# Performance work log

Hardware: AMD Instinct MI355X
Metric: run time of the kernel (lower is better)

The kernel has to match this reference:

```python
import jax, jax.numpy as jnp
import numpy as np

N = 8192          # number of nodes
D = 256           # node feature dim
OUT = 256         # output dim
AVG_DEG = 32      # target sparsity of adj (~AVG_DEG nonzeros per row)


def setup_inputs() -> dict:
    key = jax.random.key(0)
    k1, k2, k3, k4, k5 = jax.random.split(key, 5)
    node_features = jax.random.normal(k1, (N, D), dtype=jnp.float32)
    edge_features = jax.random.normal(k2, (N, N), dtype=jnp.float32)
    # sparse-ish adjacency: ~AVG_DEG nonzeros per row, stored dense (matches torch spmm math)
    u = jax.random.uniform(k3, (N, N), dtype=jnp.float32)
    adj = jnp.where(u < (AVG_DEG / N), 1.0, 0.0).astype(jnp.float32)
    stdv = 1.0 / np.sqrt(OUT)
    weight = jax.random.uniform(k4, (2 * D + 1, OUT), minval=-stdv, maxval=stdv, dtype=jnp.float32)
    bias = jax.random.uniform(k5, (OUT,), minval=-stdv, maxval=stdv, dtype=jnp.float32)
    return {"node_features": node_features, "edge_features": edge_features,
            "adj": adj, "weight": weight, "bias": bias}


def reference(node_features, edge_features, adj, weight, bias):
    # neighbor aggregation: [N,N] @ [N,D] -> [N,D]
    neighbor_node_features = adj @ node_features
    # diagonal of (adj @ edge_features) computed WITHOUT materializing the NxN product:
    # diag[i] = sum_j adj[i,j] * edge_features[j,i]
    neighbor_edge_features = jnp.einsum('ij,ji->i', adj, edge_features)[:, None]  # [N,1]
    support = jnp.concatenate(
        (node_features, neighbor_node_features, neighbor_edge_features), axis=1)  # [N, 2D+1]
    return support @ weight + bias
```

## Files before the change

### kernel.cpp

```cpp
#include <hip/hip_runtime.h>
#include <hip/hip_bf16.h>


#define NN 8192
#define DD 256
#define MAXDEG 320

typedef float f32x4 __attribute__((ext_vector_type(4)));

__global__ __launch_bounds__(256) void gemm_nf(const float* __restrict__ nf,
                                               const float* __restrict__ W,
                                               const float* __restrict__ bias,
                                               float* __restrict__ out,
                                               float* __restrict__ y2) {
    __shared__ float As[16][132];
    __shared__ float Bs[16][64];
    const int t  = threadIdx.x;
    const int bm = blockIdx.x;
    const int bn = blockIdx.y;
    const int col0 = bn * 64;
    const bool half2 = (col0 >= 256);
    const int wrow_base = half2 ? 256 : 0;
    const int wcol0 = col0 & 255;

    const int ty = t >> 4, tx = t & 15;
    const int bkk = t >> 4, bc4 = t & 15;
    const size_t abase = (size_t)bm * 128 * 256;

    float c[8][4];
#pragma unroll
    for (int i = 0; i < 8; ++i)
#pragma unroll
        for (int j = 0; j < 4; ++j) c[i][j] = 0.f;

    for (int k0 = 0; k0 < 256; k0 += 16) {
#pragma unroll
        for (int l = 0; l < 2; ++l) {
            const int idx = t + l * 256;
            const int r  = idx >> 2;
            const int c4 = idx & 3;
            float4 av = *(const float4*)(nf + abase + (size_t)r * 256 + k0 + c4 * 4);
            As[c4 * 4 + 0][r] = av.x;
            As[c4 * 4 + 1][r] = av.y;
            As[c4 * 4 + 2][r] = av.z;
            As[c4 * 4 + 3][r] = av.w;
        }
        float4 bv = *(const float4*)(W + (size_t)(wrow_base + k0 + bkk) * 256 + wcol0 + bc4 * 4);
        *(float4*)&Bs[bkk][bc4 * 4] = bv;
        __syncthreads();
#pragma unroll
        for (int k = 0; k < 16; ++k) {
            float4 a0 = *(const float4*)&As[k][ty * 8];
            float4 a1 = *(const float4*)&As[k][ty * 8 + 4];
            float4 b  = *(const float4*)&Bs[k][tx * 4];
            c[0][0] += a0.x * b.x; c[0][1] += a0.x * b.y; c[0][2] += a0.x * b.z; c[0][3] += a0.x * b.w;
            c[1][0] += a0.y * b.x; c[1][1] += a0.y * b.y; c[1][2] += a0.y * b.z; c[1][3] += a0.y * b.w;
            c[2][0] += a0.z * b.x; c[2][1] += a0.z * b.y; c[2][2] += a0.z * b.z; c[2][3] += a0.z * b.w;
            c[3][0] += a0.w * b.x; c[3][1] += a0.w * b.y; c[3][2] += a0.w * b.z; c[3][3] += a0.w * b.w;
            c[4][0] += a1.x * b.x; c[4][1] += a1.x * b.y; c[4][2] += a1.x * b.z; c[4][3] += a1.x * b.w;
            c[5][0] += a1.y * b.x; c[5][1] += a1.y * b.y; c[5][2] += a1.y * b.z; c[5][3] += a1.y * b.w;
            c[6][0] += a1.z * b.x; c[6][1] += a1.z * b.y; c[6][2] += a1.z * b.z; c[6][3] += a1.z * b.w;
            c[7][0] += a1.w * b.x; c[7][1] += a1.w * b.y; c[7][2] += a1.w * b.z; c[7][3] += a1.w * b.w;
        }
        __syncthreads();
    }

    const int row0 = bm * 128 + ty * 8;
    if (!half2) {
        float4 bv = *(const float4*)(bias + col0 + tx * 4);
#pragma unroll
        for (int r = 0; r < 8; ++r) {
            float4 v;
            v.x = c[r][0] + bv.x; v.y = c[r][1] + bv.y; v.z = c[r][2] + bv.z; v.w = c[r][3] + bv.w;
            *(float4*)(out + (size_t)(row0 + r) * 256 + col0 + tx * 4) = v;
        }
    } else {
#pragma unroll
        for (int r = 0; r < 8; ++r) {
            float4 v;
            v.x = c[r][0]; v.y = c[r][1]; v.z = c[r][2]; v.w = c[r][3];
            *(float4*)(y2 + (size_t)(row0 + r) * 256 + (col0 - 256) + tx * 4) = v;
        }
    }
}

__global__ __launch_bounds__(256, 8) void scan_agg(const float* __restrict__ adj,
                                                   const float* __restrict__ edge,
                                                   const float* __restrict__ y2,
                                                   const float* __restrict__ w3,
                                                   float* __restrict__ out) {
    __shared__ int   s_idx[MAXDEG];
    __shared__ int   s_wsum[4];
    __shared__ float s_wred[4];

    const int i = blockIdx.x;
    const int t = threadIdx.x;
    const int lane = t & 63;
    const int wv = t >> 6;

    const float wc = w3[t];

    const f32x4* arow = (const f32x4*)(adj + (size_t)i * NN);
    f32x4 va[4], vb[4];
#pragma unroll
    for (int it = 0; it < 4; ++it) va[it] = __builtin_nontemporal_load(arow + it * 256 + t);
#pragma unroll
    for (int it = 0; it < 4; ++it) vb[it] = __builtin_nontemporal_load(arow + (it + 4) * 256 + t);

    unsigned int m = 0;
#pragma unroll
    for (int it = 0; it < 4; ++it) {
        m |= (__float_as_uint(va[it].x) != 0u ? 1u : 0u) << (it * 4 + 0);
        m |= (__float_as_uint(va[it].y) != 0u ? 1u : 0u) << (it * 4 + 1);
        m |= (__float_as_uint(va[it].z) != 0u ? 1u : 0u) << (it * 4 + 2);
        m |= (__float_as_uint(va[it].w) != 0u ? 1u : 0u) << (it * 4 + 3);
    }
#pragma unroll
    for (int it = 0; it < 4; ++it) {
        m |= (__float_as_uint(vb[it].x) != 0u ? 1u : 0u) << (16 + it * 4 + 0);
        m |= (__float_as_uint(vb[it].y) != 0u ? 1u : 0u) << (16 + it * 4 + 1);
        m |= (__float_as_uint(vb[it].z) != 0u ? 1u : 0u) << (16 + it * 4 + 2);
        m |= (__float_as_uint(vb[it].w) != 0u ? 1u : 0u) << (16 + it * 4 + 3);
    }

    const int cnt_t = __popc(m);

    int incl = cnt_t;
#pragma unroll
    for (int off = 1; off < 64; off <<= 1) {
        int nb = __shfl_up(incl, off, 64);
        if (lane >= off) incl += nb;
    }
    if (lane == 63) s_wsum[wv] = incl;
    __syncthreads();

    int base = 0;
#pragma unroll
    for (int w = 0; w < 4; ++w) base += (w < wv) ? s_wsum[w] : 0;
    int cnt = s_wsum[0] + s_wsum[1] + s_wsum[2] + s_wsum[3];
    if (cnt > MAXDEG) cnt = MAXDEG;

    int pos = base + incl - cnt_t;
    unsigned int mm = m;
    while (mm) {
        const int s = __builtin_ctz(mm);
        mm &= mm - 1;
        if (pos < MAXDEG) s_idx[pos] = ((s >> 2) << 10) + (t << 2) + (s & 3);
        ++pos;
    }
    __syncthreads();

    float ev = 0.f;
    if (t < cnt) ev = edge[(size_t)s_idx[t] * NN + i];

    float acc0 = 0.f, acc1 = 0.f, acc2 = 0.f, acc3 = 0.f;
    int k = 0;
    for (; k + 3 < cnt; k += 4) {
        const int i0 = s_idx[k], i1 = s_idx[k + 1], i2 = s_idx[k + 2], i3 = s_idx[k + 3];
        acc0 += y2[(size_t)i0 * DD + t];
        acc1 += y2[(size_t)i1 * DD + t];
        acc2 += y2[(size_t)i2 * DD + t];
        acc3 += y2[(size_t)i3 * DD + t];
    }
    for (; k < cnt; ++k) acc0 += y2[(size_t)s_idx[k] * DD + t];

#pragma unroll
    for (int off = 32; off > 0; off >>= 1) ev += __shfl_down(ev, off, 64);
    if (lane == 0) s_wred[wv] = ev;
    __syncthreads();
    const float e = s_wred[0] + s_wred[1] + s_wred[2] + s_wred[3];

    const size_t o = (size_t)i * DD + t;
    out[o] = out[o] + (acc0 + acc1) + (acc2 + acc3) + e * wc;
}

extern "C" void kernel_launch(void* const* d_in, const int* in_sizes, int n_in,
                              void* d_out, int out_size, void* d_ws, size_t ws_size,
                              hipStream_t stream) {
    const float* nf   = (const float*)d_in[0];
    const float* edge = (const float*)d_in[1];
    const float* adj  = (const float*)d_in[2];
    const float* W    = (const float*)d_in[3];
    const float* bias = (const float*)d_in[4];
    float* out = (float*)d_out;
    float* y2  = (float*)d_ws;

    gemm_nf<<<dim3(64, 8), dim3(256), 0, stream>>>(nf, W, bias, out, y2);
    scan_agg<<<dim3(NN), dim3(256), 0, stream>>>(adj, edge, y2, W + (size_t)512 * 256, out);
}
```

Before: 506.5 us.

## Process multiple adjacency rows per block with double-buffered row prefetch

The scan/aggregate kernel now handles 8 rows per block instead of one. It prefetches the next adjacency row into registers while the current row's mask, scan and gather run. Shared index and reduction buffers are double-buffered by row parity. The goal is to hide the latency of the large adjacency stream, at the cost of more registers and lower occupancy (launch bound 4).

```diff
diff --git a/kernel.cpp b/kernel.cpp
--- a/kernel.cpp
+++ b/kernel.cpp
@@ -5,6 +5,7 @@
 #define NN 8192
 #define DD 256
 #define MAXDEG 320
+#define ROWS 8
 
 typedef float f32x4 __attribute__((ext_vector_type(4)));
 
@@ -84,94 +85,101 @@
     }
 }
 
-__global__ __launch_bounds__(256, 8) void scan_agg(const float* __restrict__ adj,
+__global__ __launch_bounds__(256, 4) void scan_agg(const float* __restrict__ adj,
                                                    const float* __restrict__ edge,
                                                    const float* __restrict__ y2,
                                                    const float* __restrict__ w3,
                                                    float* __restrict__ out) {
-    __shared__ int   s_idx[MAXDEG];
-    __shared__ int   s_wsum[4];
-    __shared__ float s_wred[4];
+    __shared__ int   s_idx[2][MAXDEG];
+    __shared__ int   s_wsum[2][4];
+    __shared__ float s_wred[2][4];
 
-    const int i = blockIdx.x;
     const int t = threadIdx.x;
     const int lane = t & 63;
     const int wv = t >> 6;
+    const int rbase = blockIdx.x * ROWS;
 
     const float wc = w3[t];
 
-    const f32x4* arow = (const f32x4*)(adj + (size_t)i * NN);
-    f32x4 va[4], vb[4];
+    f32x4 buf[2][8];
+    {
+        const f32x4* arow = (const f32x4*)(adj + (size_t)rbase * NN);
 #pragma unroll
-    for (int it = 0; it < 4; ++it) va[it] = __builtin_nontemporal_load(arow + it * 256 + t);
-#pragma unroll
-    for (int it = 0; it < 4; ++it) vb[it] = __builtin_nontemporal_load(arow + (it + 4) * 256 + t);
-
-    unsigned int m = 0;
-#pragma unroll
-    for (int it = 0; it < 4; ++it) {
-        m |= (__float_as_uint(va[it].x) != 0u ? 1u : 0u) << (it * 4 + 0);
-        m |= (__float_as_uint(va[it].y) != 0u ? 1u : 0u) << (it * 4 + 1);
-        m |= (__float_as_uint(va[it].z) != 0u ? 1u : 0u) << (it * 4 + 2);
-        m |= (__float_as_uint(va[it].w) != 0u ? 1u : 0u) << (it * 4 + 3);
-    }
-#pragma unroll
-    for (int it = 0; it < 4; ++it) {
-        m |= (__float_as_uint(vb[it].x) != 0u ? 1u : 0u) << (16 + it * 4 + 0);
-        m |= (__float_as_uint(vb[it].y) != 0u ? 1u : 0u) << (16 + it * 4 + 1);
-        m |= (__float_as_uint(vb[it].z) != 0u ? 1u : 0u) << (16 + it * 4 + 2);
-        m |= (__float_as_uint(vb[it].w) != 0u ? 1u : 0u) << (16 + it * 4 + 3);
+        for (int it = 0; it < 8; ++it) buf[0][it] = __builtin_nontemporal_load(arow + it * 256 + t);
     }
 
-    const int cnt_t = __popc(m);
+#pragma unroll
+    for (int r = 0; r < ROWS; ++r) {
+        const int p = r & 1;
+        const int i = rbase + r;
 
-    int incl = cnt_t;
+        if (r + 1 < ROWS) {
+            const f32x4* arow = (const f32x4*)(adj + (size_t)(i + 1) * NN);
 #pragma unroll
-    for (int off = 1; off < 64; off <<= 1) {
-        int nb = __shfl_up(incl, off, 64);
-        if (lane >= off) incl += nb;
-    }
-    if (lane == 63) s_wsum[wv] = incl;
-    __syncthreads();
+            for (int it = 0; it < 8; ++it)
+                buf[1 - p][it] = __builtin_nontemporal_load(arow + it * 256 + t);
+        }
 
-    int base = 0;
+        const size_t o = (size_t)i * DD + t;
+        const float oprev = out[o];
+
+        unsigned int m = 0;
 #pragma unroll
-    for (int w = 0; w < 4; ++w) base += (w < wv) ? s_wsum[w] : 0;
-    int cnt = s_wsum[0] + s_wsum[1] + s_wsum[2] + s_wsum[3];
-    if (cnt > MAXDEG) cnt = MAXDEG;
+        for (int it = 0; it < 8; ++it) {
+            m |= (buf[p][it].x != 0.f ? 1u : 0u) << (it * 4 + 0);
+            m |= (buf[p][it].y != 0.f ? 1u : 0u) << (it * 4 + 1);
+            m |= (buf[p][it].z != 0.f ? 1u : 0u) << (it * 4 + 2);
+            m |= (buf[p][it].w != 0.f ? 1u : 0u) << (it * 4 + 3);
+        }
+        const int cnt_t = __popc(m);
 
-    int pos = base + incl - cnt_t;
-    unsigned int mm = m;
-    while (mm) {
-        const int s = __builtin_ctz(mm);
-        mm &= mm - 1;
-        if (pos < MAXDEG) s_idx[pos] = ((s >> 2) << 10) + (t << 2) + (s & 3);
-        ++pos;
-    }
-    __syncthreads();
+        int incl = cnt_t;
+#pragma unroll
+        for (int off = 1; off < 64; off <<= 1) {
+            int nb = __shfl_up(incl, off, 64);
+            if (lane >= off) incl += nb;
+        }
+        if (lane == 63) s_wsum[p][wv] = incl;
+        __syncthreads();
 
-    float ev = 0.f;
-    if (t < cnt) ev = edge[(size_t)s_idx[t] * NN + i];
+        int base = 0;
+#pragma unroll
+        for (int w = 0; w < 4; ++w) base += (w < wv) ? s_wsum[p][w] : 0;
+        int cnt = s_wsum[p][0] + s_wsum[p][1] + s_wsum[p][2] + s_wsum[p][3];
+        if (cnt > MAXDEG) cnt = MAXDEG;
 
-    float acc0 = 0.f, acc1 = 0.f, acc2 = 0.f, acc3 = 0.f;
-    int k = 0;
-    for (; k + 3 < cnt; k += 4) {
-        const int i0 = s_idx[k], i1 = s_idx[k + 1], i2 = s_idx[k + 2], i3 = s_idx[k + 3];
-        acc0 += y2[(size_t)i0 * DD + t];
-        acc1 += y2[(size_t)i1 * DD + t];
-        acc2 += y2[(size_t)i2 * DD + t];
-        acc3 += y2[(size_t)i3 * DD + t];
-    }
-    for (; k < cnt; ++k) acc0 += y2[(size_t)s_idx[k] * DD + t];
+        int pos = base + incl - cnt_t;
+        unsigned int mm = m;
+        while (mm) {
+            const int s = __builtin_ctz(mm);
+            mm &= mm - 1;
+            if (pos < MAXDEG) s_idx[p][pos] = ((s >> 2) << 10) + (t << 2) + (s & 3);
+            ++pos;
+        }
+        __syncthreads();
+
+        float ev = 0.f;
+        if (t < cnt) ev = edge[(size_t)s_idx[p][t] * NN + i];
+
+        float acc0 = 0.f, acc1 = 0.f, acc2 = 0.f, acc3 = 0.f;
+        int k = 0;
+        for (; k + 3 < cnt; k += 4) {
+            const int i0 = s_idx[p][k], i1 = s_idx[p][k + 1], i2 = s_idx[p][k + 2], i3 = s_idx[p][k + 3];
+            acc0 += y2[(size_t)i0 * DD + t];
+            acc1 += y2[(size_t)i1 * DD + t];
+            acc2 += y2[(size_t)i2 * DD + t];
+            acc3 += y2[(size_t)i3 * DD + t];
+        }
+        for (; k < cnt; ++k) acc0 += y2[(size_t)s_idx[p][k] * DD + t];
 
 #pragma unroll
-    for (int off = 32; off > 0; off >>= 1) ev += __shfl_down(ev, off, 64);
-    if (lane == 0) s_wred[wv] = ev;
-    __syncthreads();
-    const float e = s_wred[0] + s_wred[1] + s_wred[2] + s_wred[3];
+        for (int off = 32; off > 0; off >>= 1) ev += __shfl_down(ev, off, 64);
+        if (lane == 0) s_wred[p][wv] = ev;
+        __syncthreads();
+        const float e = s_wred[p][0] + s_wred[p][1] + s_wred[p][2] + s_wred[p][3];
 
-    const size_t o = (size_t)i * DD + t;
-    out[o] = out[o] + (acc0 + acc1) + (acc2 + acc3) + e * wc;
+        out[o] = oprev + (acc0 + acc1) + (acc2 + acc3) + e * wc;
+    }
 }
 
 extern "C" void kernel_launch(void* const* d_in, const int* in_sizes, int n_in,
@@ -186,5 +194,5 @@
     float* y2  = (float*)d_ws;
 
     gemm_nf<<<dim3(64, 8), dim3(256), 0, stream>>>(nf, W, bias, out, y2);
-    scan_agg<<<dim3(NN), dim3(256), 0, stream>>>(adj, edge, y2, W + (size_t)512 * 256, out);
+    scan_agg<<<dim3(NN / ROWS), dim3(256), 0, stream>>>(adj, edge, y2, W + (size_t)512 * 256, out);
 }
```

Measured after the change: 517.3 us. 2.1% more time.

## Split adjacency scan and neighbor gather into separate kernels via index lists

Applied to the files above, without the earlier changes.

The fused scan+aggregate kernel is split into a scan_rows kernel that streams the dense adjacency and writes compact per-row neighbor index lists and counts, and a gather_agg kernel that reads those lists to gather y2 rows and edge entries. The intent is to let the bandwidth-bound adjacency stream run without gather latency interleaved, and to shrink the shared-memory list (capacity 128 instead of 320). It adds an extra launch and global round-trip for the lists, and rows with more than 128 neighbors would be silently truncated.

```diff
diff --git a/kernel.cpp b/kernel.cpp
--- a/kernel.cpp
+++ b/kernel.cpp
@@ -4,7 +4,7 @@
 
 #define NN 8192
 #define DD 256
-#define MAXDEG 320
+#define LISTCAP 128
 
 typedef float f32x4 __attribute__((ext_vector_type(4)));
 
@@ -84,45 +84,30 @@
     }
 }
 
-__global__ __launch_bounds__(256, 8) void scan_agg(const float* __restrict__ adj,
-                                                   const float* __restrict__ edge,
-                                                   const float* __restrict__ y2,
-                                                   const float* __restrict__ w3,
-                                                   float* __restrict__ out) {
-    __shared__ int   s_idx[MAXDEG];
-    __shared__ int   s_wsum[4];
-    __shared__ float s_wred[4];
+__global__ __launch_bounds__(256, 8) void scan_rows(const float* __restrict__ adj,
+                                                    int* __restrict__ lists,
+                                                    int* __restrict__ cnts) {
+    __shared__ int s_idx[LISTCAP];
+    __shared__ int s_wsum[4];
 
     const int i = blockIdx.x;
     const int t = threadIdx.x;
     const int lane = t & 63;
     const int wv = t >> 6;
 
-    const float wc = w3[t];
-
     const f32x4* arow = (const f32x4*)(adj + (size_t)i * NN);
-    f32x4 va[4], vb[4];
-#pragma unroll
-    for (int it = 0; it < 4; ++it) va[it] = __builtin_nontemporal_load(arow + it * 256 + t);
-#pragma unroll
-    for (int it = 0; it < 4; ++it) vb[it] = __builtin_nontemporal_load(arow + (it + 4) * 256 + t);
+    f32x4 v[8];
+#pragma unroll
+    for (int it = 0; it < 8; ++it) v[it] = __builtin_nontemporal_load(arow + it * 256 + t);
 
     unsigned int m = 0;
 #pragma unroll
-    for (int it = 0; it < 4; ++it) {
-        m |= (__float_as_uint(va[it].x) != 0u ? 1u : 0u) << (it * 4 + 0);
-        m |= (__float_as_uint(va[it].y) != 0u ? 1u : 0u) << (it * 4 + 1);
-        m |= (__float_as_uint(va[it].z) != 0u ? 1u : 0u) << (it * 4 + 2);
-        m |= (__float_as_uint(va[it].w) != 0u ? 1u : 0u) << (it * 4 + 3);
-    }
-#pragma unroll
-    for (int it = 0; it < 4; ++it) {
-        m |= (__float_as_uint(vb[it].x) != 0u ? 1u : 0u) << (16 + it * 4 + 0);
-        m |= (__float_as_uint(vb[it].y) != 0u ? 1u : 0u) << (16 + it * 4 + 1);
-        m |= (__float_as_uint(vb[it].z) != 0u ? 1u : 0u) << (16 + it * 4 + 2);
-        m |= (__float_as_uint(vb[it].w) != 0u ? 1u : 0u) << (16 + it * 4 + 3);
-    }
-
+    for (int it = 0; it < 8; ++it) {
+        m |= (v[it].x != 0.f ? 1u : 0u) << (it * 4 + 0);
+        m |= (v[it].y != 0.f ? 1u : 0u) << (it * 4 + 1);
+        m |= (v[it].z != 0.f ? 1u : 0u) << (it * 4 + 2);
+        m |= (v[it].w != 0.f ? 1u : 0u) << (it * 4 + 3);
+    }
     const int cnt_t = __popc(m);
 
     int incl = cnt_t;
@@ -138,16 +123,42 @@
 #pragma unroll
     for (int w = 0; w < 4; ++w) base += (w < wv) ? s_wsum[w] : 0;
     int cnt = s_wsum[0] + s_wsum[1] + s_wsum[2] + s_wsum[3];
-    if (cnt > MAXDEG) cnt = MAXDEG;
+    if (cnt > LISTCAP) cnt = LISTCAP;
 
     int pos = base + incl - cnt_t;
     unsigned int mm = m;
     while (mm) {
         const int s = __builtin_ctz(mm);
         mm &= mm - 1;
-        if (pos < MAXDEG) s_idx[pos] = ((s >> 2) << 10) + (t << 2) + (s & 3);
+        if (pos < LISTCAP) s_idx[pos] = ((s >> 2) << 10) + (t << 2) + (s & 3);
         ++pos;
     }
+    __syncthreads();
+
+    if (t == 0) cnts[i] = cnt;
+    if (t < cnt) lists[i * LISTCAP + t] = s_idx[t];
+}
+
+__global__ __launch_bounds__(256, 8) void gather_agg(const int* __restrict__ lists,
+                                                     const int* __restrict__ cnts,
+                                                     const float* __restrict__ edge,
+                                                     const float* __restrict__ y2,
+                                                     const float* __restrict__ w3,
+                                                     float* __restrict__ out) {
+    __shared__ int   s_idx[LISTCAP];
+    __shared__ float s_wred[4];
+
+    const int i = blockIdx.x;
+    const int t = threadIdx.x;
+    const int lane = t & 63;
+    const int wv = t >> 6;
+
+    const int cnt = cnts[i];
+    if (t < cnt) s_idx[t] = lists[i * LISTCAP + t];
+
+    const size_t o = (size_t)i * DD + t;
+    const float oprev = out[o];
+    const float wc = w3[t];
     __syncthreads();
 
     float ev = 0.f;
@@ -170,8 +181,7 @@
     __syncthreads();
     const float e = s_wred[0] + s_wred[1] + s_wred[2] + s_wred[3];
 
-    const size_t o = (size_t)i * DD + t;
-    out[o] = out[o] + (acc0 + acc1) + (acc2 + acc3) + e * wc;
+    out[o] = oprev + (acc0 + acc1) + (acc2 + acc3) + e * wc;
 }
 
 extern "C" void kernel_launch(void* const* d_in, const int* in_sizes, int n_in,
@@ -183,8 +193,12 @@
     const float* W    = (const float*)d_in[3];
     const float* bias = (const float*)d_in[4];
     float* out = (float*)d_out;
-    float* y2  = (float*)d_ws;
+
+    float* y2   = (float*)d_ws;
+    int*   cnts = (int*)((char*)d_ws + (size_t)NN * DD * 4);
+    int*   lists = cnts + NN;
 
     gemm_nf<<<dim3(64, 8), dim3(256), 0, stream>>>(nf, W, bias, out, y2);
-    scan_agg<<<dim3(NN), dim3(256), 0, stream>>>(adj, edge, y2, W + (size_t)512 * 256, out);
-}
+    scan_rows<<<dim3(NN), dim3(256), 0, stream>>>(adj, lists, cnts);
+    gather_agg<<<dim3(NN), dim3(256), 0, stream>>>(lists, cnts, edge, y2, W + (size_t)512 * 256, out);
+}
```

Measured after the change: 510.5 us. No clear change (+0.8%).
